# Performance work log

Measured on AMD Instinct MI355X. Metric: run time of the kernel, lower is better.

The kernel has to match this reference:

```python
import jax, jax.numpy as jnp
import numpy as np

POS_WEIGHT = 5.0

def setup_inputs() -> dict:
    key = jax.random.key(0)
    k1, k2, k3, k4 = jax.random.split(key, 4)
    B, S, P = 128, 32768, 65536
    preds = jax.random.normal(k1, (B, S), dtype=jnp.float32)
    targets = jax.random.randint(k2, (B, S), 0, 2, dtype=jnp.int32)
    # monotone (sorted) warping-path indices, like a DTW alignment path
    pi = jnp.sort(jax.random.randint(k3, (B, P), 0, S), axis=1)
    pj = jnp.sort(jax.random.randint(k4, (B, P), 0, S), axis=1)
    paths = jnp.stack([pi, pj], axis=-1).astype(jnp.int64)  # [B, P, 2]
    return {"preds": preds, "targets": targets, "paths": paths}

def _per_batch_loss(pred, target, path):
    # pred: [S], target: [S] int, path: [P, 2] of (i, j) pairs
    S = pred.shape[0]
    P = path.shape[0]
    pi, pj = path[:, 0], path[:, 1]
    steps = jnp.arange(P)
    # first step index k at which each target position j appears in the path
    first_k = jax.ops.segment_min(steps, pj, num_segments=S)  # [S]
    is_first = steps == first_k[pj]                            # first occurrence of j
    hit = (target[pj] == 1) & is_first                         # first-match to an SoS target
    # scatter-first-write: gt[i] = 1 for the matched pred positions
    gt = jnp.zeros((S,), dtype=pred.dtype).at[pi].max(hit.astype(pred.dtype))
    # BCEWithLogitsLoss with pos_weight, mean reduction (numerically stable)
    loss = -(POS_WEIGHT * gt * jax.nn.log_sigmoid(pred)
             + (1.0 - gt) * jax.nn.log_sigmoid(-pred))
    return loss.mean()

def reference(preds, targets, paths):
    per_batch = jax.vmap(_per_batch_loss)(preds, targets, paths)  # [B]
    return per_batch.mean()  # sum over batch / batch_size
```

## Files before the change

### kernel.cpp

```cpp
#include <hip/hip_runtime.h>

#define NB 128
#define NS 32768
#define NP 65536
#define POS_W 5.0f

constexpr int MASK_WORDS = (NB * NS) / 32;
constexpr int WPB        = NS / 32;
constexpr int LOSS_BLOCKS = 512;
constexpr int CHUNK4      = (NB * NS / 4) / LOSS_BLOCKS;
constexpr int MWPC        = CHUNK4 / 8;


__global__ __launch_bounds__(256)
void tbit_kernel(const int* __restrict__ targets, unsigned int* __restrict__ tb) {
    constexpr int NSEG = NB * NS / 64;
    const int lane = threadIdx.x & 63;
    const int wid  = (blockIdx.x * blockDim.x + threadIdx.x) >> 6;
    const int nw   = (gridDim.x * blockDim.x) >> 6;
    for (int s = wid; s < NSEG; s += nw) {
        const unsigned long long m = __ballot(targets[(size_t)s * 64 + lane] != 0);
        if (lane == 0)       tb[s * 2]     = (unsigned int)m;
        else if (lane == 32) tb[s * 2 + 1] = (unsigned int)(m >> 32);
    }
}

template <int QPB>
__global__ __launch_bounds__(512)
void gt_kernel(const int* __restrict__ pw, const unsigned int* __restrict__ tbits_g,
               unsigned int* __restrict__ pmask) {
    __shared__ unsigned int tbits[WPB];
    __shared__ unsigned int gbits[WPB];

    const int is64 = (pw[2 * (size_t)NP - 1] == 0);

    const int q    = blockIdx.x;
    const int b    = blockIdx.y;
    const int tid  = threadIdx.x;
    const int lane = tid & 63;
    const int wbase = tid & ~63;

    tbits[tid]       = tbits_g[(size_t)b * WPB + tid];
    tbits[tid + 512] = tbits_g[(size_t)b * WPB + tid + 512];
    gbits[tid]       = 0u;
    gbits[tid + 512] = 0u;
    __syncthreads();

    constexpr int STEPS = NP / QPB;
    const int    k0    = q * STEPS;
    const size_t sbase = (size_t)b * NP + k0;
    const int4*  p4    = (const int4*)pw;

    if (!is64) {
        constexpr int NIT = STEPS / 1024;
        constexpr int NCH = (NIT + 7) / 8;
        const size_t pb = sbase >> 1;
        int bval = -1;
        if (lane < NIT) {
            const int kf = k0 + (lane * 512 + wbase) * 2;
            if (kf != 0) bval = pw[2 * ((size_t)b * NP + kf) - 1];
        }
        #pragma unroll
        for (int ch = 0; ch < NCH; ++ch) {
            int4 a[8];
            #pragma unroll
            for (int j = 0; j < 8; ++j) a[j] = p4[pb + (ch * 8 + j) * 512 + tid];
            #pragma unroll
            for (int j = 0; j < 8; ++j) {
                const int it = ch * 8 + j;
                const int pi0 = a[j].x, pj0 = a[j].y, pi1 = a[j].z, pj1 = a[j].w;
                const int pl = __shfl_up(pj1, 1);
                const int bv = __shfl(bval, it);
                const int prev = (lane == 0) ? bv : pl;
                const bool f0 = (pj0 != prev);
                const bool f1 = (pj1 != pj0);
                if (f0 && ((tbits[pj0 >> 5] >> (pj0 & 31)) & 1u))
                    atomicOr(&gbits[pi0 >> 5], 1u << (pi0 & 31));
                if (f1 && ((tbits[pj1 >> 5] >> (pj1 & 31)) & 1u))
                    atomicOr(&gbits[pi1 >> 5], 1u << (pi1 & 31));
            }
        }
    } else {
        constexpr int NIT = STEPS / 512;
        constexpr int NCH = (NIT + 7) / 8;
        int bval = -1;
        if (lane < NIT) {
            const int kf = k0 + lane * 512 + wbase;
            if (kf != 0) bval = pw[4 * ((size_t)b * NP + kf) - 2];
        }
        #pragma unroll
        for (int ch = 0; ch < NCH; ++ch) {
            int4 a[8];
            #pragma unroll
            for (int j = 0; j < 8; ++j) a[j] = p4[sbase + (ch * 8 + j) * 512 + tid];
            #pragma unroll
            for (int j = 0; j < 8; ++j) {
                const int it = ch * 8 + j;
                const int pi = a[j].x, pj = a[j].z;
                const int pl = __shfl_up(pj, 1);
                const int bv = __shfl(bval, it);
                const int prev = (lane == 0) ? bv : pl;
                if ((pj != prev) && ((tbits[pj >> 5] >> (pj & 31)) & 1u))
                    atomicOr(&gbits[pi >> 5], 1u << (pi & 31));
            }
        }
    }
    __syncthreads();

    unsigned int* dst = pmask + (size_t)q * MASK_WORDS + (size_t)b * WPB;
    dst[tid]       = gbits[tid];
    dst[tid + 512] = gbits[tid + 512];
}

template <int QPB>
__global__ __launch_bounds__(256)
void loss_kernel(const float* __restrict__ preds, const unsigned int* __restrict__ pmask,
                 float* __restrict__ partials) {
    __shared__ unsigned int mmask[MWPC];
    const int tid = threadIdx.x;
    const int cb4 = blockIdx.x * CHUNK4;
    const int mb  = blockIdx.x * MWPC;

    unsigned int mw = 0u;
    #pragma unroll
    for (int q = 0; q < QPB; ++q)
        mw |= pmask[(size_t)q * MASK_WORDS + mb + tid];
    mmask[tid] = mw;
    __syncthreads();

    float acc = 0.f;
    #pragma unroll
    for (int it = 0; it < CHUNK4 / 256; ++it) {
        const int li = it * 256 + tid;
        const float4 x = reinterpret_cast<const float4*>(preds)[cb4 + li];
        const unsigned int m = mmask[li >> 3] >> ((li & 7) * 4);
        const float xs[4] = {x.x, x.y, x.z, x.w};
        #pragma unroll
        for (int j = 0; j < 4; ++j) {
            const float v = xs[j];
            const float t = __logf(1.f + __expf(-fabsf(v)));
            const float sp_pos = t + fmaxf(v, 0.f);
            const float sp_neg = sp_pos - v;
            acc += ((m >> j) & 1u) ? POS_W * sp_neg : sp_pos;
        }
    }
    for (int off = 32; off; off >>= 1) acc += __shfl_down(acc, off);
    __shared__ float sacc[4];
    const int wave = tid >> 6, lane = tid & 63;
    if (lane == 0) sacc[wave] = acc;
    __syncthreads();
    if (tid == 0) {
        float s = 0.f;
        #pragma unroll
        for (int w = 0; w < 4; ++w) s += sacc[w];
        partials[blockIdx.x] = s;
    }
}

__global__ __launch_bounds__(256)
void final_kernel(const float* __restrict__ partials, float* __restrict__ out) {
    float acc = 0.f;
    for (int i = threadIdx.x; i < LOSS_BLOCKS; i += 256) acc += partials[i];
    for (int off = 32; off; off >>= 1) acc += __shfl_down(acc, off);
    __shared__ float sacc[4];
    const int wave = threadIdx.x >> 6, lane = threadIdx.x & 63;
    if (lane == 0) sacc[wave] = acc;
    __syncthreads();
    if (threadIdx.x == 0) {
        float s = 0.f;
        #pragma unroll
        for (int w = 0; w < 4; ++w) s += sacc[w];
        out[0] = s * (1.0f / ((float)NB * (float)NS));
    }
}

extern "C" void kernel_launch(void* const* d_in, const int* in_sizes, int n_in,
                              void* d_out, int out_size, void* d_ws, size_t ws_size,
                              hipStream_t stream) {
    const float* preds   = (const float*)d_in[0];
    const int*   targets = (const int*)d_in[1];
    const int*   paths_w = (const int*)d_in[2];
    float*       out     = (float*)d_out;

    int qpb = 8;
    while (qpb > 2 &&
           ws_size < (size_t)(1 + qpb) * MASK_WORDS * 4 + (size_t)LOSS_BLOCKS * 4)
        qpb >>= 1;

    unsigned int* tbits_g  = (unsigned int*)d_ws;
    unsigned int* pmask    = tbits_g + MASK_WORDS;
    float*        partials = (float*)((char*)d_ws +
                              (size_t)(1 + qpb) * MASK_WORDS * 4);

    tbit_kernel<<<1024, 256, 0, stream>>>(targets, tbits_g);

    dim3 g1(qpb, NB);
    switch (qpb) {
        case 8:
            gt_kernel<8><<<g1, 512, 0, stream>>>(paths_w, tbits_g, pmask);
            loss_kernel<8><<<LOSS_BLOCKS, 256, 0, stream>>>(preds, pmask, partials);
            break;
        case 4:
            gt_kernel<4><<<g1, 512, 0, stream>>>(paths_w, tbits_g, pmask);
            loss_kernel<4><<<LOSS_BLOCKS, 256, 0, stream>>>(preds, pmask, partials);
            break;
        default:
            gt_kernel<2><<<g1, 512, 0, stream>>>(paths_w, tbits_g, pmask);
            loss_kernel<2><<<LOSS_BLOCKS, 256, 0, stream>>>(preds, pmask, partials);
            break;
    }

    final_kernel<<<1, 256, 0, stream>>>(partials, out);
}
```

Measured before the change: 33.62 us.

## Stage path loads via global_load_lds DMA with per-wave contiguous double buffering

In the int32-path branch of gt_kernel, each wave now owns a contiguous slice of path steps and streams it through LDS with global_load_lds DMA in a two-stage double buffer. The first-occurrence check carries the previous pj across rows with a wave shuffle instead of per-iteration boundary loads. The aim is to overlap global loads with the bit-test and atomicOr work and to cut register pressure from the eight int4 prefetch registers. It adds 32KB of LDS per block, which may lower occupancy. The schedule is hardcoded for 8 rows per wave, so it only holds when QPB is 8.

New measurement: 37.43 us. +11.3%, slower.

```diff
diff --git a/kernel.cpp b/kernel.cpp
--- a/kernel.cpp
+++ b/kernel.cpp
@@ -11,6 +11,16 @@
 constexpr int CHUNK4      = (NB * NS / 4) / LOSS_BLOCKS;
 constexpr int MWPC        = CHUNK4 / 8;
 
+
+__device__ __forceinline__ void dma16(const void* g, void* l) {
+    __builtin_amdgcn_global_load_lds(
+        (const __attribute__((address_space(1))) void*)g,
+        (__attribute__((address_space(3))) void*)l,
+        16, 0, 0);
+}
+#define GT_WAIT(N) do { \
+    asm volatile("s_waitcnt vmcnt(" #N ")" ::: "memory"); \
+    __builtin_amdgcn_sched_barrier(0); } while (0)
 
 __global__ __launch_bounds__(256)
 void tbit_kernel(const int* __restrict__ targets, unsigned int* __restrict__ tb) {
@@ -31,6 +41,7 @@
                unsigned int* __restrict__ pmask) {
     __shared__ unsigned int tbits[WPB];
     __shared__ unsigned int gbits[WPB];
+    __shared__ int4 stage[8][256];
 
     const int is64 = (pw[2 * (size_t)NP - 1] == 0);
 
@@ -38,7 +49,7 @@
     const int b    = blockIdx.y;
     const int tid  = threadIdx.x;
     const int lane = tid & 63;
-    const int wbase = tid & ~63;
+    const int w    = tid >> 6;
 
     tbits[tid]       = tbits_g[(size_t)b * WPB + tid];
     tbits[tid + 512] = tbits_g[(size_t)b * WPB + tid + 512];
@@ -52,37 +63,45 @@
     const int4*  p4    = (const int4*)pw;
 
     if (!is64) {
-        constexpr int NIT = STEPS / 1024;
-        constexpr int NCH = (NIT + 7) / 8;
-        const size_t pb = sbase >> 1;
-        int bval = -1;
-        if (lane < NIT) {
-            const int kf = k0 + (lane * 512 + wbase) * 2;
-            if (kf != 0) bval = pw[2 * ((size_t)b * NP + kf) - 1];
-        }
-        #pragma unroll
-        for (int ch = 0; ch < NCH; ++ch) {
-            int4 a[8];
+        constexpr int WSTEPS = STEPS / 8;
+        const int    kw    = k0 + w * WSTEPS;
+        const size_t ibase = (sbase >> 1) + (size_t)w * (WSTEPS / 2);
+
+        int carry = -1;
+        if (kw != 0) carry = pw[2 * ((size_t)b * NP + kw) - 1];
+
+        auto proc2 = [&](int h) {
             #pragma unroll
-            for (int j = 0; j < 8; ++j) a[j] = p4[pb + (ch * 8 + j) * 512 + tid];
-            #pragma unroll
-            for (int j = 0; j < 8; ++j) {
-                const int it = ch * 8 + j;
-                const int pi0 = a[j].x, pj0 = a[j].y, pi1 = a[j].z, pj1 = a[j].w;
+            for (int rr = 0; rr < 2; ++rr) {
+                const int4 a = stage[w][h * 128 + rr * 64 + lane];
+                const int pi0 = a.x, pj0 = a.y, pi1 = a.z, pj1 = a.w;
                 const int pl = __shfl_up(pj1, 1);
-                const int bv = __shfl(bval, it);
-                const int prev = (lane == 0) ? bv : pl;
+                const int prev = (lane == 0) ? carry : pl;
                 const bool f0 = (pj0 != prev);
                 const bool f1 = (pj1 != pj0);
                 if (f0 && ((tbits[pj0 >> 5] >> (pj0 & 31)) & 1u))
                     atomicOr(&gbits[pi0 >> 5], 1u << (pi0 & 31));
                 if (f1 && ((tbits[pj1 >> 5] >> (pj1 & 31)) & 1u))
                     atomicOr(&gbits[pi1 >> 5], 1u << (pi1 & 31));
+                carry = __shfl(pj1, 63);
             }
-        }
+        };
+        auto issue2 = [&](int r, int h) {
+            dma16(p4 + ibase + (size_t)r * 64 + lane, &stage[w][h * 128]);
+            dma16(p4 + ibase + (size_t)(r + 1) * 64 + lane, &stage[w][h * 128 + 64]);
+        };
+
+        issue2(0, 0); issue2(2, 1);
+        GT_WAIT(2);  proc2(0);
+        issue2(4, 0);
+        GT_WAIT(2);  proc2(1);
+        issue2(6, 1);
+        GT_WAIT(2);  proc2(0);
+        GT_WAIT(0);  proc2(1);
     } else {
         constexpr int NIT = STEPS / 512;
         constexpr int NCH = (NIT + 7) / 8;
+        const int wbase = tid & ~63;
         int bval = -1;
         if (lane < NIT) {
             const int kf = k0 + lane * 512 + wbase;
```

## Fix gt_kernel at 4 quarters, 256 threads with double-buffered path loads

Applied to the files above, without the earlier changes.

Replaces the templated per-batch path scan with a fixed configuration of four quarters per batch and 256-thread blocks, dropping the runtime workspace-size selection. The path loads are double-buffered across two int4 register arrays so that the next chunk's global loads are issued while the current chunk is processed. This is meant to hide the global-load latency in the scatter phase. In exchange it uses more registers and removes the fallback for smaller workspaces.

Measured after the change: 36.75 us. 9.3% more time.

```diff
diff --git a/kernel.cpp b/kernel.cpp
--- a/kernel.cpp
+++ b/kernel.cpp
@@ -7,6 +7,7 @@
 
 constexpr int MASK_WORDS = (NB * NS) / 32;
 constexpr int WPB        = NS / 32;
+constexpr int QPB        = 4;
 constexpr int LOSS_BLOCKS = 512;
 constexpr int CHUNK4      = (NB * NS / 4) / LOSS_BLOCKS;
 constexpr int MWPC        = CHUNK4 / 8;
@@ -25,8 +26,7 @@
     }
 }
 
-template <int QPB>
-__global__ __launch_bounds__(512)
+__global__ __launch_bounds__(256)
 void gt_kernel(const int* __restrict__ pw, const unsigned int* __restrict__ tbits_g,
                unsigned int* __restrict__ pmask) {
     __shared__ unsigned int tbits[WPB];
@@ -40,10 +40,11 @@
     const int lane = tid & 63;
     const int wbase = tid & ~63;
 
-    tbits[tid]       = tbits_g[(size_t)b * WPB + tid];
-    tbits[tid + 512] = tbits_g[(size_t)b * WPB + tid + 512];
-    gbits[tid]       = 0u;
-    gbits[tid + 512] = 0u;
+    #pragma unroll
+    for (int r = 0; r < 4; ++r) {
+        tbits[r * 256 + tid] = tbits_g[(size_t)b * WPB + r * 256 + tid];
+        gbits[r * 256 + tid] = 0u;
+    }
     __syncthreads();
 
     constexpr int STEPS = NP / QPB;
@@ -52,67 +53,89 @@
     const int4*  p4    = (const int4*)pw;
 
     if (!is64) {
-        constexpr int NIT = STEPS / 1024;
-        constexpr int NCH = (NIT + 7) / 8;
+        constexpr int NIT = STEPS / (256 * 2);
         const size_t pb = sbase >> 1;
+
         int bval = -1;
         if (lane < NIT) {
-            const int kf = k0 + (lane * 512 + wbase) * 2;
+            const int kf = k0 + (lane * 256 + wbase) * 2;
             if (kf != 0) bval = pw[2 * ((size_t)b * NP + kf) - 1];
         }
-        #pragma unroll
-        for (int ch = 0; ch < NCH; ++ch) {
-            int4 a[8];
-            #pragma unroll
-            for (int j = 0; j < 8; ++j) a[j] = p4[pb + (ch * 8 + j) * 512 + tid];
-            #pragma unroll
-            for (int j = 0; j < 8; ++j) {
-                const int it = ch * 8 + j;
-                const int pi0 = a[j].x, pj0 = a[j].y, pi1 = a[j].z, pj1 = a[j].w;
-                const int pl = __shfl_up(pj1, 1);
-                const int bv = __shfl(bval, it);
-                const int prev = (lane == 0) ? bv : pl;
-                const bool f0 = (pj0 != prev);
-                const bool f1 = (pj1 != pj0);
-                if (f0 && ((tbits[pj0 >> 5] >> (pj0 & 31)) & 1u))
-                    atomicOr(&gbits[pi0 >> 5], 1u << (pi0 & 31));
-                if (f1 && ((tbits[pj1 >> 5] >> (pj1 & 31)) & 1u))
-                    atomicOr(&gbits[pi1 >> 5], 1u << (pi1 & 31));
+
+        int4 a0[8], a1[8];
+        #define GT_ISSUE(buf, ch) \
+            _Pragma("unroll") \
+            for (int j = 0; j < 8; ++j) buf[j] = p4[pb + ((ch) * 8 + j) * 256 + tid];
+        #define GT_PROC(buf, ch) \
+            _Pragma("unroll") \
+            for (int j = 0; j < 8; ++j) { \
+                const int it = (ch) * 8 + j; \
+                const int pi0 = buf[j].x, pj0 = buf[j].y; \
+                const int pi1 = buf[j].z, pj1 = buf[j].w; \
+                const int pl = __shfl_up(pj1, 1); \
+                const int bv = __shfl(bval, it); \
+                const int prev = (lane == 0) ? bv : pl; \
+                const bool f0 = (pj0 != prev); \
+                const bool f1 = (pj1 != pj0); \
+                if (f0 && ((tbits[pj0 >> 5] >> (pj0 & 31)) & 1u)) \
+                    atomicOr(&gbits[pi0 >> 5], 1u << (pi0 & 31)); \
+                if (f1 && ((tbits[pj1 >> 5] >> (pj1 & 31)) & 1u)) \
+                    atomicOr(&gbits[pi1 >> 5], 1u << (pi1 & 31)); \
             }
-        }
+
+        GT_ISSUE(a0, 0)
+        GT_ISSUE(a1, 1)
+        GT_PROC(a0, 0)
+        GT_ISSUE(a0, 2)
+        GT_PROC(a1, 1)
+        GT_ISSUE(a1, 3)
+        GT_PROC(a0, 2)
+        GT_PROC(a1, 3)
+        #undef GT_ISSUE
+        #undef GT_PROC
     } else {
-        constexpr int NIT = STEPS / 512;
-        constexpr int NCH = (NIT + 7) / 8;
+        constexpr int NIT = STEPS / 256;
         int bval = -1;
-        if (lane < NIT) {
-            const int kf = k0 + lane * 512 + wbase;
+        {
+            const int kf = k0 + lane * 256 + wbase;
             if (kf != 0) bval = pw[4 * ((size_t)b * NP + kf) - 2];
         }
-        #pragma unroll
-        for (int ch = 0; ch < NCH; ++ch) {
-            int4 a[8];
-            #pragma unroll
-            for (int j = 0; j < 8; ++j) a[j] = p4[sbase + (ch * 8 + j) * 512 + tid];
-            #pragma unroll
-            for (int j = 0; j < 8; ++j) {
-                const int it = ch * 8 + j;
-                const int pi = a[j].x, pj = a[j].z;
-                const int pl = __shfl_up(pj, 1);
-                const int bv = __shfl(bval, it);
-                const int prev = (lane == 0) ? bv : pl;
-                if ((pj != prev) && ((tbits[pj >> 5] >> (pj & 31)) & 1u))
-                    atomicOr(&gbits[pi >> 5], 1u << (pi & 31));
+
+        int4 a0[8], a1[8];
+        #define GT_ISSUE64(buf, ch) \
+            _Pragma("unroll") \
+            for (int j = 0; j < 8; ++j) buf[j] = p4[sbase + ((ch) * 8 + j) * 256 + tid];
+        #define GT_PROC64(buf, ch) \
+            _Pragma("unroll") \
+            for (int j = 0; j < 8; ++j) { \
+                const int it = (ch) * 8 + j; \
+                const int pi = buf[j].x, pj = buf[j].z; \
+                const int pl = __shfl_up(pj, 1); \
+                const int bv = __shfl(bval, it); \
+                const int prev = (lane == 0) ? bv : pl; \
+                if ((pj != prev) && ((tbits[pj >> 5] >> (pj & 31)) & 1u)) \
+                    atomicOr(&gbits[pi >> 5], 1u << (pi & 31)); \
             }
-        }
+
+        GT_ISSUE64(a0, 0)
+        GT_ISSUE64(a1, 1)
+        #pragma unroll
+        for (int ch = 0; ch < 8; ch += 2) {
+            GT_PROC64(a0, ch)
+            if (ch + 2 < 8) GT_ISSUE64(a0, ch + 2)
+            GT_PROC64(a1, ch + 1)
+            if (ch + 3 < 8) GT_ISSUE64(a1, ch + 3)
+        }
+        #undef GT_ISSUE64
+        #undef GT_PROC64
     }
     __syncthreads();
 
     unsigned int* dst = pmask + (size_t)q * MASK_WORDS + (size_t)b * WPB;
-    dst[tid]       = gbits[tid];
-    dst[tid + 512] = gbits[tid + 512];
-}
-
-template <int QPB>
+    #pragma unroll
+    for (int r = 0; r < 4; ++r) dst[r * 256 + tid] = gbits[r * 256 + tid];
+}
+
 __global__ __launch_bounds__(256)
 void loss_kernel(const float* __restrict__ preds, const unsigned int* __restrict__ pmask,
                  float* __restrict__ partials) {
@@ -182,33 +205,16 @@
     const int*   paths_w = (const int*)d_in[2];
     float*       out     = (float*)d_out;
 
-    int qpb = 8;
-    while (qpb > 2 &&
-           ws_size < (size_t)(1 + qpb) * MASK_WORDS * 4 + (size_t)LOSS_BLOCKS * 4)
-        qpb >>= 1;
-
     unsigned int* tbits_g  = (unsigned int*)d_ws;
     unsigned int* pmask    = tbits_g + MASK_WORDS;
     float*        partials = (float*)((char*)d_ws +
-                              (size_t)(1 + qpb) * MASK_WORDS * 4);
+                              (size_t)(1 + QPB) * MASK_WORDS * 4);
 
     tbit_kernel<<<1024, 256, 0, stream>>>(targets, tbits_g);
 
-    dim3 g1(qpb, NB);
-    switch (qpb) {
-        case 8:
-            gt_kernel<8><<<g1, 512, 0, stream>>>(paths_w, tbits_g, pmask);
-            loss_kernel<8><<<LOSS_BLOCKS, 256, 0, stream>>>(preds, pmask, partials);
-            break;
-        case 4:
-            gt_kernel<4><<<g1, 512, 0, stream>>>(paths_w, tbits_g, pmask);
-            loss_kernel<4><<<LOSS_BLOCKS, 256, 0, stream>>>(preds, pmask, partials);
-            break;
-        default:
-            gt_kernel<2><<<g1, 512, 0, stream>>>(paths_w, tbits_g, pmask);
-            loss_kernel<2><<<LOSS_BLOCKS, 256, 0, stream>>>(preds, pmask, partials);
-            break;
-    }
-
+    dim3 g1(QPB, NB);
+    gt_kernel<<<g1, 256, 0, stream>>>(paths_w, tbits_g, pmask);
+
+    loss_kernel<<<LOSS_BLOCKS, 256, 0, stream>>>(preds, pmask, partials);
     final_kernel<<<1, 256, 0, stream>>>(partials, out);
 }
```
